# Optimization experiments

Hardware: AMD Instinct MI355X
Metric: run time of the kernel (lower is better)

Reference implementation:

```python
import jax, jax.numpy as jnp
import numpy as np

T, B, N, C, H = 4, 32, 256, 384, 8
D = C // H
TAU = 2.0
EPS = 1e-5
SCALE = C ** -0.5

# --- surrogate-gradient spike (spikingjelly Sigmoid surrogate, alpha=4) ---
@jax.custom_vjp
def spike(x):
    return (x >= 0.0).astype(x.dtype)

def _spike_fwd(x):
    return spike(x), x

def _spike_bwd(x, g):
    s = jax.nn.sigmoid(4.0 * x)
    return (g * 4.0 * s * (1.0 - s),)

spike.defvjp(_spike_fwd, _spike_bwd)

def lif(x):
    # MultiStepLIFNode: v' = v + (x - (v - v_reset))/tau, v_reset=0, v_th=1, hard reset, detach_reset
    def step(v, xt):
        h = v + (xt - v) / TAU
        s = spike(h - 1.0)
        v_next = h * (1.0 - jax.lax.stop_gradient(s))
        return v_next, s
    _, spikes = jax.lax.scan(step, jnp.zeros_like(x[0]), x)
    return spikes

def bn_c(x, gamma, beta, mean, var):
    # BatchNorm1d over channel dim C in eval mode; x: [TB, N, C]
    return (x - mean) * (gamma * jax.lax.rsqrt(var + EPS)) + beta

def setup_inputs() -> dict:
    key = jax.random.key(0)
    ks = jax.random.split(key, 10)
    x = jax.random.normal(ks[0], (T, B, N, C), jnp.float32)
    def w(k):
        return jax.random.normal(k, (C, C), jnp.float32) * (C ** -0.5)
    def bn(k):
        kg, kb, km, kv = jax.random.split(k, 4)
        return jnp.stack([
            1.0 + 0.1 * jax.random.normal(kg, (C,), jnp.float32),
            0.1 * jax.random.normal(kb, (C,), jnp.float32),
            0.1 * jax.random.normal(km, (C,), jnp.float32),
            jax.random.uniform(kv, (C,), jnp.float32, 0.5, 1.5),
        ])  # [gamma, beta, running_mean, running_var]
    rel_table = 0.02 * jax.random.normal(ks[9], (2 * N - 1, H), jnp.float32)
    return {
        "x": x,
        "w_q": w(ks[1]), "w_k": w(ks[2]), "w_v": w(ks[3]), "w_p": w(ks[4]),
        "bn_q": bn(ks[5]), "bn_k": bn(ks[6]), "bn_v": bn(ks[7]), "bn_p": bn(ks[8]),
        "rel_table": rel_table,
    }

def reference(x, w_q, w_k, w_v, w_p, bn_q, bn_k, bn_v, bn_p, rel_table):
    xf = x.reshape(T * B, N, C)

    def branch(w, bnp):
        y = bn_c(xf @ w.T, *bnp).reshape(T, B, N, C)
        y = lif(y)
        return y.reshape(T, B, N, H, D).transpose(0, 1, 3, 2, 4)  # [T,B,H,N,D]

    q = branch(w_q, bn_q)
    k = branch(w_k, bn_k)
    v = branch(w_v, bn_v)

    scores = jnp.einsum('tbhnd,tbhmd->tbhnm', q, k)  # [T,B,H,N,N]
    # relative bias: idx[i,j] = i - j + N - 1
    idx = jnp.arange(N)[:, None] - jnp.arange(N)[None, :] + N - 1
    bias = rel_table[idx]  # [N,N,H]
    scores = scores + bias.transpose(2, 0, 1)[None, None]

    out = jnp.einsum('tbhnm,tbhmd->tbhnd', scores, v) * SCALE
    out = out.transpose(0, 1, 3, 2, 4).reshape(T, B, N, C)
    out = lif(out)  # attn_lif

    y = bn_c(out.reshape(T * B, N, C) @ w_p.T, *bn_p).reshape(T, B, N, C)
    return lif(y)  # proj_lif; dropout is eval-mode identity
```

## Files before the change

kernel.cpp:

```cpp
#include <hip/hip_runtime.h>
#include <stdint.h>

#define T_ 4
#define B_ 32
#define N_ 256
#define C_ 384
#define H_ 8
#define D_ 48
#define ROWS (B_*N_)
#define SCALE_F 0.051031036307982884f

#define QS_OFF 0u
#define KS_OFF 25165824u
#define VS_OFF 50331648u
#define AS_OFF 75497472u
#define WH_OFF 0u
#define WM_OFF 294912u
#define WL_OFF 589824u

typedef __bf16 bf16x8 __attribute__((ext_vector_type(8)));
typedef float  f32x4  __attribute__((ext_vector_type(4)));

__device__ __forceinline__ void split3(float s, uint32_t& h, uint32_t& m, uint32_t& l) {
    uint32_t u  = __float_as_uint(s);
    uint32_t hu = u & 0xffff0000u;
    float r1 = s - __uint_as_float(hu);
    uint32_t u1 = __float_as_uint(r1);
    uint32_t mu = u1 & 0xffff0000u;
    float r2 = r1 - __uint_as_float(mu);
    h = hu >> 16; m = mu >> 16; l = __float_as_uint(r2) >> 16;
}

__global__ void k_wsplit3(const float* __restrict__ wq, const float* __restrict__ wk,
                          const float* __restrict__ wv, uint16_t* __restrict__ out)
{
    const int br = blockIdx.y;
    const float* __restrict__ w = (br==0)? wq : (br==1)? wk : wv;
    const int idx = blockIdx.x*256 + threadIdx.x;
    uint32_t h, m, l;
    split3(w[idx], h, m, l);
    uint16_t* base = out + (size_t)br*442368;
    base[idx] = (uint16_t)h;
    base[147456 + idx] = (uint16_t)m;
    base[294912 + idx] = (uint16_t)l;
}

#define SA 104

__global__ __launch_bounds__(256, 3) void k_qkv_v6(
    const float* __restrict__ x, const uint16_t* __restrict__ wbr,
    const float* __restrict__ bnq, const float* __restrict__ bnk, const float* __restrict__ bnv,
    uint16_t* __restrict__ qs, uint16_t* __restrict__ ks, uint16_t* __restrict__ vs)
{
    const int cb = blockIdx.x;
    const int branch = cb / 3;
    const int ct = cb - branch*3;
    const int c0 = ct * 128;
    const int bn0 = blockIdx.y * 32;
    const float* __restrict__ bnp_ = (branch==0)? bnq : (branch==1)? bnk : bnv;
    uint16_t* __restrict__ outp = (branch==0)? qs : (branch==1)? ks : vs;
    const uint16_t* __restrict__ wpl = wbr + (size_t)branch*442368;

    __shared__ __align__(16) uint16_t At[128][SA];
    __shared__ __align__(16) uint16_t Bp[3][128][32];

    const int tid  = threadIdx.x;
    const int wv   = tid >> 6;
    const int lane = tid & 63;
    const int l15  = lane & 15;
    const int quad = lane >> 4;
    const int q8   = quad * 8;
    const int rg   = wv >> 1;
    const int wcol = (wv & 1) * 64;
    const int wvu  = __builtin_amdgcn_readfirstlane(wv);

    f32x4 acc[4][4];
    #pragma unroll
    for (int it=0; it<4; ++it)
        #pragma unroll
        for (int jt=0; jt<4; ++jt) acc[it][jt] = (f32x4){0.f,0.f,0.f,0.f};

    const int trow = tid >> 1, half = tid & 1;
    const int tA = trow >> 5, bnlA = trow & 31;
    const float* xrow = x + ((size_t)(tA*ROWS + bn0 + bnlA))*C_ + half*16;

    const uint16_t* bsrc[6];
    uint16_t* bdst[6];
    #pragma unroll
    for (int s=0; s<6; ++s) {
        const int gi = wvu*6 + s;
        const int p = gi >> 3, chunk = gi & 7;
        bsrc[s] = wpl + (size_t)p*147456
                + (size_t)(c0 + chunk*16 + (lane>>2))*C_ + (lane&3)*8;
        bdst[s] = &Bp[p][chunk*16][0];
    }

    float fe[16];
    #pragma unroll
    for (int s=0; s<4; ++s)
        *(float4*)&fe[4*s] = *(const float4*)(xrow + 4*s);

    for (int kt=0; kt<12; ++kt) {
        const int k0 = kt*32;
        __syncthreads();
        #pragma unroll
        for (int s=0; s<6; ++s) {
            __builtin_amdgcn_global_load_lds(
                (const __attribute__((address_space(1))) uint32_t*)(bsrc[s] + k0),
                (__attribute__((address_space(3))) uint32_t*)(bdst[s]),
                16, 0, 0);
        }
        {
            uint32_t hw[8], mw[8], lw[8];
            #pragma unroll
            for (int i=0; i<8; ++i) {
                const float s0 = fe[2*i], s1 = fe[2*i+1];
                const uint32_t h0 = __float_as_uint(s0) & 0xffff0000u;
                const uint32_t h1 = __float_as_uint(s1) & 0xffff0000u;
                const float r0 = s0 - __uint_as_float(h0);
                const float r1 = s1 - __uint_as_float(h1);
                const uint32_t m0 = __float_as_uint(r0) & 0xffff0000u;
                const uint32_t m1 = __float_as_uint(r1) & 0xffff0000u;
                const float p0 = r0 - __uint_as_float(m0);
                const float p1 = r1 - __uint_as_float(m1);
                hw[i] = (h0>>16) | h1;
                mw[i] = (m0>>16) | m1;
                lw[i] = (__float_as_uint(p0)>>16) | (__float_as_uint(p1) & 0xffff0000u);
            }
            *(uint4*)&At[trow][ 0 + half*16]     = make_uint4(hw[0],hw[1],hw[2],hw[3]);
            *(uint4*)&At[trow][ 0 + half*16 + 8] = make_uint4(hw[4],hw[5],hw[6],hw[7]);
            *(uint4*)&At[trow][32 + half*16]     = make_uint4(mw[0],mw[1],mw[2],mw[3]);
            *(uint4*)&At[trow][32 + half*16 + 8] = make_uint4(mw[4],mw[5],mw[6],mw[7]);
            *(uint4*)&At[trow][64 + half*16]     = make_uint4(lw[0],lw[1],lw[2],lw[3]);
            *(uint4*)&At[trow][64 + half*16 + 8] = make_uint4(lw[4],lw[5],lw[6],lw[7]);
        }
        __syncthreads();

        if (kt < 11) {
            const float* xn = xrow + (kt+1)*32;
            #pragma unroll
            for (int s=0; s<4; ++s)
                *(float4*)&fe[4*s] = *(const float4*)(xn + 4*s);
        }

        bf16x8 af[4][3];
        #pragma unroll
        for (int it=0; it<4; ++it) {
            const uint16_t* ar = &At[rg*64 + it*16 + l15][q8];
            af[it][0] = *(const bf16x8*)(ar);
            af[it][1] = *(const bf16x8*)(ar + 32);
            af[it][2] = *(const bf16x8*)(ar + 64);
        }
        #pragma unroll
        for (int jt=0; jt<4; ++jt) {
            const int brow = wcol + jt*16 + l15;
            const bf16x8 b0 = *(const bf16x8*)&Bp[0][brow][q8];
            const bf16x8 b1 = *(const bf16x8*)&Bp[1][brow][q8];
            const bf16x8 b2 = *(const bf16x8*)&Bp[2][brow][q8];
            #pragma unroll
            for (int it=0; it<4; ++it) {
                f32x4 a = acc[it][jt];
                a = __builtin_amdgcn_mfma_f32_16x16x32_bf16(af[it][0], b0, a, 0,0,0);
                a = __builtin_amdgcn_mfma_f32_16x16x32_bf16(af[it][0], b1, a, 0,0,0);
                a = __builtin_amdgcn_mfma_f32_16x16x32_bf16(af[it][1], b0, a, 0,0,0);
                a = __builtin_amdgcn_mfma_f32_16x16x32_bf16(af[it][0], b2, a, 0,0,0);
                a = __builtin_amdgcn_mfma_f32_16x16x32_bf16(af[it][1], b1, a, 0,0,0);
                a = __builtin_amdgcn_mfma_f32_16x16x32_bf16(af[it][2], b0, a, 0,0,0);
                acc[it][jt] = a;
            }
        }
    }

    __syncthreads();
    float* vex = (float*)&At[0][0];

    #define STORE_SP(tt, sp) do { \
        if (branch == 2) { \
            const int h2 = cg / 48, dd = cg - h2*48; \
            const int bng = bn0 + bnl; \
            outp[((((size_t)(tt)*B_ + (bng>>8))*H_ + h2)*D_ + dd)*N_ + (bng&255)] = (sp); \
        } else { \
            outp[((size_t)((tt)*ROWS + bn0 + bnl))*C_ + cg] = (sp); \
        } \
    } while(0)

    if (rg == 0) {
        #pragma unroll
        for (int jt=0; jt<4; ++jt) {
            const int cl = wcol + jt*16 + l15;
            const int cg = c0 + cl;
            const float g = bnp_[cg], be = bnp_[C_+cg], mu = bnp_[2*C_+cg], va = bnp_[3*C_+cg];
            const float scl = g * (float)(1.0 / sqrt((double)(va + 1e-5f)));
            #pragma unroll
            for (int a=0; a<2; ++a)
                #pragma unroll
                for (int r=0; r<4; ++r) {
                    const int bnl = a*16 + quad*4 + r;
                    const float y0 = (acc[a  ][jt][r] - mu)*scl + be;
                    const float y1 = (acc[a+2][jt][r] - mu)*scl + be;
                    float v = 0.f;
                    float h = v + (y0 - v)*0.5f;
                    STORE_SP(0, (h >= 1.0f) ? (uint16_t)0x3f80 : (uint16_t)0);
                    v = (h >= 1.0f) ? 0.f : h;
                    h = v + (y1 - v)*0.5f;
                    STORE_SP(1, (h >= 1.0f) ? (uint16_t)0x3f80 : (uint16_t)0);
                    v = (h >= 1.0f) ? 0.f : h;
                    vex[bnl*128 + cl] = v;
                }
        }
    }
    __syncthreads();
    if (rg == 1) {
        #pragma unroll
        for (int jt=0; jt<4; ++jt) {
            const int cl = wcol + jt*16 + l15;
            const int cg = c0 + cl;
            const float g = bnp_[cg], be = bnp_[C_+cg], mu = bnp_[2*C_+cg], va = bnp_[3*C_+cg];
            const float scl = g * (float)(1.0 / sqrt((double)(va + 1e-5f)));
            #pragma unroll
            for (int a=0; a<2; ++a)
                #pragma unroll
                for (int r=0; r<4; ++r) {
                    const int bnl = a*16 + quad*4 + r;
                    const float y2 = (acc[a  ][jt][r] - mu)*scl + be;
                    const float y3 = (acc[a+2][jt][r] - mu)*scl + be;
                    float v = vex[bnl*128 + cl];
                    float h = v + (y2 - v)*0.5f;
                    STORE_SP(2, (h >= 1.0f) ? (uint16_t)0x3f80 : (uint16_t)0);
                    v = (h >= 1.0f) ? 0.f : h;
                    h = v + (y3 - v)*0.5f;
                    STORE_SP(3, (h >= 1.0f) ? (uint16_t)0x3f80 : (uint16_t)0);
                }
        }
    }
    #undef STORE_SP
}

__global__ __launch_bounds__(256, 2) void k_attn(
    const uint16_t* __restrict__ qs, const uint16_t* __restrict__ ks, const uint16_t* __restrict__ vs,
    const float* __restrict__ rel, uint16_t* __restrict__ as_)
{
    const int bh = blockIdx.x;
    const int b = bh >> 3, h = bh & 7;
    const int i0 = blockIdx.y * 128;

    __shared__ __align__(16) uint16_t qt[128][72];
    __shared__ __align__(16) uint16_t kt[32][72];
    __shared__ __align__(16) uint16_t vT[48][40];
    __shared__ __align__(16) uint16_t sh[3][128][40];
    __shared__ float tab_s[384];

    const int tid  = threadIdx.x;
    const int wv_  = tid >> 6;
    const int lane = tid & 63;
    const int l15  = lane & 15;
    const int quad = lane >> 4;
    const int w32  = wv_ * 32;
    const int q8   = quad * 8;

    for (int l = tid; l < 383; l += 256) tab_s[l] = rel[(size_t)(i0 + l)*H_ + h];
    {
        const uint4 z = make_uint4(0,0,0,0);
        { const int row = tid >> 1, seg = tid & 1;
          *(uint4*)&qt[row][48 + seg*8] = z; }
        if (tid < 64) { const int row = tid >> 1, seg = tid & 1;
          *(uint4*)&kt[row][48 + seg*8] = z; }
    }

    float vst[2][3][4];
    #pragma unroll
    for (int a=0;a<2;++a)
        #pragma unroll
        for (int e=0;e<3;++e)
            #pragma unroll
            for (int r=0;r<4;++r) vst[a][e][r]=0.f;

    for (int t=0; t<4; ++t) {
        const int tb = t*B_ + b;
        __syncthreads();
        #pragma unroll
        for (int rep=0; rep<3; ++rep) {
            const int l = rep*256 + tid;
            const int row = l / 6, seg = l - 6*row;
            *(uint4*)&qt[row][seg*8] =
                *(const uint4*)(qs + ((size_t)(tb*N_ + i0 + row))*C_ + h*D_ + seg*8);
        }

        f32x4 pacc[2][3];
        #pragma unroll
        for (int a=0;a<2;++a)
            #pragma unroll
            for (int e=0;e<3;++e) pacc[a][e] = (f32x4){0.f,0.f,0.f,0.f};

        for (int j0 = 0; j0 < 256; j0 += 32) {
            __syncthreads();
            if (tid < 192) {
                const int row = tid / 6, seg = tid - 6*row;
                *(uint4*)&kt[row][seg*8] =
                    *(const uint4*)(ks + ((size_t)(tb*N_ + j0 + row))*C_ + h*D_ + seg*8);
            } else {
                const int l = tid - 192;
                #pragma unroll
                for (int rep=0; rep<3; ++rep) {
                    const int e = rep*64 + l;
                    const int d = e >> 2, seg = e & 3;
                    *(uint4*)&vT[d][seg*8] =
                        *(const uint4*)(vs + (((size_t)(tb*H_ + h))*D_ + d)*N_ + j0 + seg*8);
                }
            }
            __syncthreads();

            f32x4 sacc[2][2];
            #pragma unroll
            for (int a=0;a<2;++a)
                #pragma unroll
                for (int c2=0;c2<2;++c2) sacc[a][c2] = (f32x4){0.f,0.f,0.f,0.f};
            bf16x8 qa[2][2];
            #pragma unroll
            for (int it=0; it<2; ++it)
                #pragma unroll
                for (int ks_=0; ks_<2; ++ks_)
                    qa[it][ks_] = *(const bf16x8*)&qt[w32 + it*16 + l15][ks_*32 + q8];
            #pragma unroll
            for (int jt=0; jt<2; ++jt) {
                #pragma unroll
                for (int ks_=0; ks_<2; ++ks_) {
                    const bf16x8 kb = *(const bf16x8*)&kt[jt*16 + l15][ks_*32 + q8];
                    #pragma unroll
                    for (int it=0; it<2; ++it)
                        sacc[it][jt] = __builtin_amdgcn_mfma_f32_16x16x32_bf16(
                            qa[it][ks_], kb, sacc[it][jt], 0, 0, 0);
                }
            }

            #pragma unroll
            for (int it=0; it<2; ++it)
                #pragma unroll
                for (int jt=0; jt<2; ++jt) {
                    const int jl = jt*16 + l15;
                    const int jg = j0 + jl;
                    #pragma unroll
                    for (int r=0; r<4; ++r) {
                        const int il = w32 + it*16 + quad*4 + r;
                        const float s = sacc[it][jt][r] + tab_s[il - jg + 255];
                        uint32_t hh, mm, ll;
                        split3(s, hh, mm, ll);
                        sh[0][il][jl] = (uint16_t)hh;
                        sh[1][il][jl] = (uint16_t)mm;
                        sh[2][il][jl] = (uint16_t)ll;
                    }
                }

            bf16x8 vb[3];
            #pragma unroll
            for (int dt=0; dt<3; ++dt)
                vb[dt] = *(const bf16x8*)&vT[dt*16 + l15][q8];
            #pragma unroll
            for (int it=0; it<2; ++it)
                #pragma unroll
                for (int p=0; p<3; ++p) {
                    const bf16x8 sa = *(const bf16x8*)&sh[p][w32 + it*16 + l15][q8];
                    #pragma unroll
                    for (int dt=0; dt<3; ++dt)
                        pacc[it][dt] = __builtin_amdgcn_mfma_f32_16x16x32_bf16(
                            sa, vb[dt], pacc[it][dt], 0, 0, 0);
                }
        }

        #pragma unroll
        for (int it=0; it<2; ++it)
            #pragma unroll
            for (int dt=0; dt<3; ++dt)
                #pragma unroll
                for (int r=0; r<4; ++r) {
                    const float xin = pacc[it][dt][r] * SCALE_F;
                    float v = vst[it][dt][r];
                    const float hh = v + (xin - v)*0.5f;
                    const uint16_t sp = (hh >= 1.0f) ? (uint16_t)0x3f80 : (uint16_t)0;
                    vst[it][dt][r] = (hh >= 1.0f) ? 0.f : hh;
                    const int ig = i0 + w32 + it*16 + quad*4 + r;
                    const int c  = h*D_ + dt*16 + l15;
                    as_[((size_t)(tb*N_ + ig))*C_ + c] = sp;
                }
    }
}

__global__ void k_wsplit(const float* __restrict__ wp,
                         uint16_t* __restrict__ wh, uint16_t* __restrict__ wm,
                         uint16_t* __restrict__ wl)
{
    const int idx = blockIdx.x*256 + threadIdx.x;
    uint32_t h, m, l;
    split3(wp[idx], h, m, l);
    wh[idx] = (uint16_t)h; wm[idx] = (uint16_t)m; wl[idx] = (uint16_t)l;
}

__global__ __launch_bounds__(256, 2) void k_proj(
    const uint16_t* __restrict__ as_,
    const uint16_t* __restrict__ wh, const uint16_t* __restrict__ wm,
    const uint16_t* __restrict__ wl,
    const float* __restrict__ bnp, float* __restrict__ out)
{
    const int r0 = blockIdx.x * 64;
    const int c0 = blockIdx.y * 96;

    __shared__ __align__(16) uint16_t At[4][64][40];
    __shared__ __align__(16) uint16_t Bt[3][96][40];

    const int tid  = threadIdx.x;
    const int wv_  = tid >> 6;
    const int lane = tid & 63;
    const int l15  = lane & 15;
    const int quad = lane >> 4;
    const int q8   = quad * 8;

    f32x4 acc[4][6];
    #pragma unroll
    for (int t=0;t<4;++t)
        #pragma unroll
        for (int nt=0;nt<6;++nt) acc[t][nt] = (f32x4){0.f,0.f,0.f,0.f};

    for (int kstep=0; kstep<12; ++kstep) {
        const int k0 = kstep*32;
        __syncthreads();
        #pragma unroll
        for (int rep=0; rep<4; ++rep) {
            const int l = rep*256 + tid;
            const int t = l >> 8, row = (l >> 2) & 63, seg = l & 3;
            *(uint4*)&At[t][row][seg*8] =
                *(const uint4*)(as_ + ((size_t)(t*ROWS + r0 + row))*C_ + k0 + seg*8);
        }
        for (int l = tid; l < 1152; l += 256) {
            const int p = l / 384, rem = l - 384*p;
            const int c = rem >> 2, seg = rem & 3;
            const uint16_t* src = (p==0)? wh : (p==1)? wm : wl;
            *(uint4*)&Bt[p][c][seg*8] =
                *(const uint4*)(src + (size_t)(c0 + c)*C_ + k0 + seg*8);
        }
        __syncthreads();

        bf16x8 af[4];
        #pragma unroll
        for (int t=0;t<4;++t)
            af[t] = *(const bf16x8*)&At[t][wv_*16 + l15][q8];
        #pragma unroll
        for (int nt=0; nt<6; ++nt) {
            #pragma unroll
            for (int p=0; p<3; ++p) {
                const bf16x8 bf_ = *(const bf16x8*)&Bt[p][nt*16 + l15][q8];
                #pragma unroll
                for (int t=0;t<4;++t)
                    acc[t][nt] = __builtin_amdgcn_mfma_f32_16x16x32_bf16(
                        af[t], bf_, acc[t][nt], 0, 0, 0);
            }
        }
    }

    #pragma unroll
    for (int nt=0; nt<6; ++nt) {
        const int c = c0 + nt*16 + l15;
        const float g = bnp[c], be = bnp[C_+c], mu = bnp[2*C_+c], va = bnp[3*C_+c];
        const float scl = g * (float)(1.0 / sqrt((double)(va + 1e-5f)));
        #pragma unroll
        for (int r=0; r<4; ++r) {
            const int rg = r0 + wv_*16 + quad*4 + r;
            float v = 0.f;
            #pragma unroll
            for (int t=0; t<4; ++t) {
                const float y  = (acc[t][nt][r] - mu)*scl + be;
                const float hh = v + (y - v)*0.5f;
                const float sp = (hh >= 1.0f) ? 1.0f : 0.f;
                v = (hh >= 1.0f) ? 0.f : hh;
                out[((size_t)(t*ROWS + rg))*C_ + c] = sp;
            }
        }
    }
}

extern "C" void kernel_launch(void* const* d_in, const int* in_sizes, int n_in,
                              void* d_out, int out_size, void* d_ws, size_t ws_size,
                              hipStream_t stream) {
    const float* x   = (const float*)d_in[0];
    const float* wq  = (const float*)d_in[1];
    const float* wk  = (const float*)d_in[2];
    const float* wv  = (const float*)d_in[3];
    const float* wp  = (const float*)d_in[4];
    const float* bnq = (const float*)d_in[5];
    const float* bnk = (const float*)d_in[6];
    const float* bnv = (const float*)d_in[7];
    const float* bnp = (const float*)d_in[8];
    const float* rel = (const float*)d_in[9];
    float* out = (float*)d_out;
    uint8_t* ws = (uint8_t*)d_ws;
    uint16_t* qs  = (uint16_t*)(ws + QS_OFF);
    uint16_t* ks  = (uint16_t*)(ws + KS_OFF);
    uint16_t* vs  = (uint16_t*)(ws + VS_OFF);
    uint16_t* as_ = (uint16_t*)(ws + AS_OFF);
    uint16_t* wbr = (uint16_t*)(ws + AS_OFF);
    uint16_t* wh  = (uint16_t*)(ws + WH_OFF);
    uint16_t* wm  = (uint16_t*)(ws + WM_OFF);
    uint16_t* wl  = (uint16_t*)(ws + WL_OFF);

    k_wsplit3<<<dim3(576, 3), 256, 0, stream>>>(wq, wk, wv, wbr);
    k_qkv_v6 <<<dim3(9, 256), 256, 0, stream>>>(x, wbr, bnq, bnk, bnv, qs, ks, vs);
    k_attn   <<<dim3(256, 2), 256, 0, stream>>>(qs, ks, vs, rel, as_);
    k_wsplit <<<dim3(576),    256, 0, stream>>>(wp, wh, wm, wl);
    k_proj   <<<dim3(128, 4), 256, 0, stream>>>(as_, wh, wm, wl, bnp, out);
}
```

Measured before the change: 375.7 us.

## Transpose score MFMA for packed LDS stores; use direct global-to-LDS loads in projection

```diff
diff --git a/kernel.cpp b/kernel.cpp
--- a/kernel.cpp
+++ b/kernel.cpp
@@ -328,28 +328,33 @@
                     const bf16x8 kb = *(const bf16x8*)&kt[jt*16 + l15][ks_*32 + q8];
                     #pragma unroll
                     for (int it=0; it<2; ++it)
-                        sacc[it][jt] = __builtin_amdgcn_mfma_f32_16x16x32_bf16(
-                            qa[it][ks_], kb, sacc[it][jt], 0, 0, 0);
-                }
-            }
-
-            #pragma unroll
-            for (int it=0; it<2; ++it)
+                        sacc[jt][it] = __builtin_amdgcn_mfma_f32_16x16x32_bf16(
+                            kb, qa[it][ks_], sacc[jt][it], 0, 0, 0);
+                }
+            }
+
+            #pragma unroll
+            for (int it=0; it<2; ++it) {
+                const int il = w32 + it*16 + l15;
                 #pragma unroll
                 for (int jt=0; jt<2; ++jt) {
-                    const int jl = jt*16 + l15;
-                    const int jg = j0 + jl;
+                    uint32_t wpk[3][2];
                     #pragma unroll
                     for (int r=0; r<4; ++r) {
-                        const int il = w32 + it*16 + quad*4 + r;
-                        const float s = sacc[it][jt][r] + tab_s[il - jg + 255];
+                        const int jl = jt*16 + quad*4 + r;
+                        const int jg = j0 + jl;
+                        const float s = sacc[jt][it][r] + tab_s[il - jg + 255];
                         uint32_t hh, mm, ll;
                         split3(s, hh, mm, ll);
-                        sh[0][il][jl] = (uint16_t)hh;
-                        sh[1][il][jl] = (uint16_t)mm;
-                        sh[2][il][jl] = (uint16_t)ll;
+                        if (r & 1) { wpk[0][r>>1] |= hh<<16; wpk[1][r>>1] |= mm<<16; wpk[2][r>>1] |= ll<<16; }
+                        else       { wpk[0][r>>1]  = hh;     wpk[1][r>>1]  = mm;     wpk[2][r>>1]  = ll;   }
                     }
-                }
+                    const int jb = jt*16 + quad*4;
+                    #pragma unroll
+                    for (int p=0; p<3; ++p)
+                        *(uint2*)&sh[p][il][jb] = make_uint2(wpk[p][0], wpk[p][1]);
+                }
+            }
 
             bf16x8 vb[3];
             #pragma unroll
@@ -395,17 +400,15 @@
     wh[idx] = (uint16_t)h; wm[idx] = (uint16_t)m; wl[idx] = (uint16_t)l;
 }
 
-__global__ __launch_bounds__(256, 2) void k_proj(
-    const uint16_t* __restrict__ as_,
-    const uint16_t* __restrict__ wh, const uint16_t* __restrict__ wm,
-    const uint16_t* __restrict__ wl,
+__global__ __launch_bounds__(256, 3) void k_proj_v2(
+    const uint16_t* __restrict__ as_, const uint16_t* __restrict__ wh,
     const float* __restrict__ bnp, float* __restrict__ out)
 {
     const int r0 = blockIdx.x * 64;
     const int c0 = blockIdx.y * 96;
 
-    __shared__ __align__(16) uint16_t At[4][64][40];
-    __shared__ __align__(16) uint16_t Bt[3][96][40];
+    __shared__ __align__(16) uint16_t Ap[4][64][32];
+    __shared__ __align__(16) uint16_t Bp[3][96][32];
 
     const int tid  = threadIdx.x;
     const int wv_  = tid >> 6;
@@ -413,6 +416,28 @@
     const int l15  = lane & 15;
     const int quad = lane >> 4;
     const int q8   = quad * 8;
+    const int wvu  = __builtin_amdgcn_readfirstlane(wv_);
+
+    const uint16_t* srcs[9];
+    uint16_t* dsts[9];
+    int nch = 0;
+    for (int s = 0; s < 9; ++s) {
+        const int g = wvu + 4*s;
+        if (g < 34) {
+            if (g < 16) {
+                const int t = g >> 2, rgp = g & 3;
+                srcs[nch] = as_ + ((size_t)(t*ROWS + r0 + rgp*16 + (lane>>2)))*C_ + (lane&3)*8;
+                dsts[nch] = &Ap[t][rgp*16][0];
+            } else {
+                const int g2 = g - 16;
+                const int p = g2 / 6, rgp = g2 - 6*p;
+                srcs[nch] = wh + (size_t)p*147456
+                          + (size_t)(c0 + rgp*16 + (lane>>2))*C_ + (lane&3)*8;
+                dsts[nch] = &Bp[p][rgp*16][0];
+            }
+            ++nch;
+        }
+    }
 
     f32x4 acc[4][6];
     #pragma unroll
@@ -423,31 +448,23 @@
     for (int kstep=0; kstep<12; ++kstep) {
         const int k0 = kstep*32;
         __syncthreads();
-        #pragma unroll
-        for (int rep=0; rep<4; ++rep) {
-            const int l = rep*256 + tid;
-            const int t = l >> 8, row = (l >> 2) & 63, seg = l & 3;
-            *(uint4*)&At[t][row][seg*8] =
-                *(const uint4*)(as_ + ((size_t)(t*ROWS + r0 + row))*C_ + k0 + seg*8);
-        }
-        for (int l = tid; l < 1152; l += 256) {
-            const int p = l / 384, rem = l - 384*p;
-            const int c = rem >> 2, seg = rem & 3;
-            const uint16_t* src = (p==0)? wh : (p==1)? wm : wl;
-            *(uint4*)&Bt[p][c][seg*8] =
-                *(const uint4*)(src + (size_t)(c0 + c)*C_ + k0 + seg*8);
+        for (int s = 0; s < nch; ++s) {
+            __builtin_amdgcn_global_load_lds(
+                (const __attribute__((address_space(1))) uint32_t*)(srcs[s] + k0),
+                (__attribute__((address_space(3))) uint32_t*)(dsts[s]),
+                16, 0, 0);
         }
         __syncthreads();
 
         bf16x8 af[4];
         #pragma unroll
         for (int t=0;t<4;++t)
-            af[t] = *(const bf16x8*)&At[t][wv_*16 + l15][q8];
+            af[t] = *(const bf16x8*)&Ap[t][wv_*16 + l15][q8];
         #pragma unroll
         for (int nt=0; nt<6; ++nt) {
             #pragma unroll
             for (int p=0; p<3; ++p) {
-                const bf16x8 bf_ = *(const bf16x8*)&Bt[p][nt*16 + l15][q8];
+                const bf16x8 bf_ = *(const bf16x8*)&Bp[p][nt*16 + l15][q8];
                 #pragma unroll
                 for (int t=0;t<4;++t)
                     acc[t][nt] = __builtin_amdgcn_mfma_f32_16x16x32_bf16(
@@ -505,5 +522,5 @@
     k_qkv_v6 <<<dim3(9, 256), 256, 0, stream>>>(x, wbr, bnq, bnk, bnv, qs, ks, vs);
     k_attn   <<<dim3(256, 2), 256, 0, stream>>>(qs, ks, vs, rel, as_);
     k_wsplit <<<dim3(576),    256, 0, stream>>>(wp, wh, wm, wl);
-    k_proj   <<<dim3(128, 4), 256, 0, stream>>>(as_, wh, wm, wl, bnp, out);
-}
+    k_proj_v2<<<dim3(128, 4), 256, 0, stream>>>(as_, wh, bnp, out);
+}
```

Result: slower. 394.9 us (+5.1%).
